# Optimization experiments

Measured on AMD Instinct MI355X. Metric: run time of the kernel, lower is better.

The kernel has to match this reference:

```python
import jax, jax.numpy as jnp
import numpy as np

C_M, C_Z, C = 256, 128, 32
LN_EPS = 1e-5


def setup_inputs() -> dict:
    key = jax.random.key(0)
    ks = jax.random.split(key, 9)
    S, R = 128, 384  # N_seq, N_res
    m = jax.random.normal(ks[0], (S, R, C_M), dtype=jnp.float32)
    ln_g = jnp.ones((C_M,), jnp.float32)
    ln_b = jnp.zeros((C_M,), jnp.float32)
    w1 = jax.random.normal(ks[1], (C_M, C), jnp.float32) / np.sqrt(C_M)
    b1 = jnp.zeros((C,), jnp.float32)
    w2 = jax.random.normal(ks[2], (C_M, C), jnp.float32) / np.sqrt(C_M)
    b2 = jnp.zeros((C,), jnp.float32)
    w_out = jax.random.normal(ks[3], (C * C, C_Z), jnp.float32) / np.sqrt(C * C)
    b_out = jnp.zeros((C_Z,), jnp.float32)
    return {"m": m, "ln_g": ln_g, "ln_b": ln_b, "w1": w1, "b1": b1,
            "w2": w2, "b2": b2, "w_out": w_out, "b_out": b_out}


def reference(m, ln_g, ln_b, w1, b1, w2, b2, w_out, b_out):
    S, R, _ = m.shape
    # LayerNorm over c_m
    mu = jnp.mean(m, axis=-1, keepdims=True)
    var = jnp.var(m, axis=-1, keepdims=True)
    mn = (m - mu) * jax.lax.rsqrt(var + LN_EPS) * ln_g + ln_b
    a = mn @ w1 + b1  # (S, R, c)
    b = mn @ w2 + b2  # (S, R, c)
    # outer product summed over N_seq: out[i,j,x,y] = sum_s a[s,i,x] b[s,j,y]
    o = jnp.einsum('six,sjy->ijxy', a, b)  # (R, R, c, c)
    o = o.reshape(R, R, C * C) @ w_out + b_out  # (R, R, c_z)
    return o / S
```

## Files before the change

### kernel.cpp

```cpp
#include <hip/hip_runtime.h>
#include <hip/hip_bf16.h>

#define R_RES 384
#define S_SEQ 128
#define CM 256
#define CC 32
#define CZ 128

typedef __attribute__((ext_vector_type(8))) short bf16x8;
typedef __attribute__((ext_vector_type(4))) float f32x4;
typedef __attribute__((ext_vector_type(16))) float f32x16;
typedef __attribute__((ext_vector_type(4))) int i32x4;

__device__ __forceinline__ short tobf16(float f) {
    union { __hip_bfloat16 h; short s; } u;
    u.h = __float2bfloat16(f);
    return u.s;
}

__global__ void k_transpose_wout(const float* __restrict__ w_out, short* __restrict__ wbTf) {
    __shared__ float t[64][65];
    int k0 = blockIdx.x * 64;
    int z0 = blockIdx.y * 64;
    int tid = threadIdx.x;
    int c = tid & 63, rg = tid >> 6;
#pragma unroll
    for (int rr = 0; rr < 16; ++rr) {
        int kk = rg * 16 + rr;
        t[kk][c] = w_out[(size_t)(k0 + kk) * CZ + z0 + c];
    }
    __syncthreads();
#pragma unroll
    for (int l = 0; l < 2; ++l) {
        int id = l * 256 + tid;
        int f = id >> 6;
        int ksl = f >> 1, fzl = f & 1;
        int ln = id & 63;
        int zl = fzl * 32 + (ln & 31);
        int kl = ksl * 16 + (ln >> 5) * 8;
        bf16x8 pk;
#pragma unroll
        for (int j = 0; j < 8; ++j) pk[j] = tobf16(t[kl + j][zl]);
        size_t fz = blockIdx.y * 2 + fzl;
        size_t ks16 = blockIdx.x * 4 + ksl;
        *(bf16x8*)(wbTf + ((fz * 64 + ks16) * 64 + ln) * 8) = pk;
    }
}

__global__ void k_pack_w12(const float* __restrict__ w1, const float* __restrict__ w2,
                           short* __restrict__ wcT) {
    int idx = blockIdx.x * 256 + threadIdx.x;
    int k = idx >> 6, n = idx & 63;
    float v = (n < 32) ? w1[k * CC + n] : w2[k * CC + (n - 32)];
    wcT[n * CM + k] = tobf16(v);
}

__global__ __launch_bounds__(256) void k_ln_proj(
    const float* __restrict__ M, const float* __restrict__ ln_g, const float* __restrict__ ln_b,
    const float* __restrict__ b1, const float* __restrict__ b2,
    const short* __restrict__ wcT, short* __restrict__ aTf, short* __restrict__ bTf) {
    __shared__ short mnb[64 * 256];
    __shared__ short ab_s[2][32 * 72];
    int r = blockIdx.x >> 1;
    int s0 = (blockIdx.x & 1) * 64;
    int tid = threadIdx.x, lane = tid & 63, w = tid >> 6;
    int g = lane >> 4, r16 = lane & 15;
    float4 gv = *(const float4*)(ln_g + lane * 4);
    float4 bv = *(const float4*)(ln_b + lane * 4);
    for (int it = 0; it < 16; ++it) {
        int sl = it * 4 + w;
        float4 v = *(const float4*)(M + ((size_t)(s0 + sl) * R_RES + r) * CM + lane * 4);
        float sum = v.x + v.y + v.z + v.w;
        float sq = v.x * v.x + v.y * v.y + v.z * v.z + v.w * v.w;
#pragma unroll
        for (int off = 32; off; off >>= 1) {
            sum += __shfl_xor(sum, off);
            sq  += __shfl_xor(sq, off);
        }
        float mu = sum * (1.0f / 256.0f);
        float var = sq * (1.0f / 256.0f) - mu * mu;
        float rstd = rsqrtf(var + 1e-5f);
        short4 mnp;
        mnp.x = tobf16((v.x - mu) * rstd * gv.x + bv.x);
        mnp.y = tobf16((v.y - mu) * rstd * gv.y + bv.y);
        mnp.z = tobf16((v.z - mu) * rstd * gv.z + bv.z);
        mnp.w = tobf16((v.w - mu) * rstd * gv.w + bv.w);
        int byte = sl * 512 + lane * 8;
        byte ^= ((sl & 7) << 4);
        *(short4*)((char*)mnb + byte) = mnp;
    }
    __syncthreads();
    f32x4 acc[4] = {{0,0,0,0},{0,0,0,0},{0,0,0,0},{0,0,0,0}};
    int srow = w * 16 + r16;
#pragma unroll
    for (int ks = 0; ks < 8; ++ks) {
        int byte = srow * 512 + ks * 64 + g * 16;
        byte ^= ((srow & 7) << 4);
        bf16x8 af = *(const bf16x8*)((const char*)mnb + byte);
#pragma unroll
        for (int nt = 0; nt < 4; ++nt) {
            bf16x8 bf = *(const bf16x8*)(wcT + (nt * 16 + r16) * CM + ks * 32 + g * 8);
            acc[nt] = __builtin_amdgcn_mfma_f32_16x16x32_bf16(af, bf, acc[nt], 0, 0, 0);
        }
    }
#pragma unroll
    for (int nt = 0; nt < 4; ++nt) {
        int n = nt * 16 + r16;
        int x = n & 31, sel = n >> 5;
        float bias = sel ? b2[x] : b1[x];
#pragma unroll
        for (int rr = 0; rr < 4; ++rr) {
            int sl = w * 16 + g * 4 + rr;
            ab_s[sel][x * 72 + sl] = tobf16(acc[nt][rr] + bias);
        }
    }
    __syncthreads();
    int piece = tid >> 6;
    int fl = piece >> 1, kl = piece & 1;
    int ln = tid & 63;
    int x = fl * 16 + (ln & 15);
    int s_loc = kl * 32 + (ln >> 4) * 8;
    i32x4 va = *(const i32x4*)((const char*)ab_s[0] + (x * 72 + s_loc) * 2);
    i32x4 vb = *(const i32x4*)((const char*)ab_s[1] + (x * 72 + s_loc) * 2);
    size_t off = ((((size_t)r * 2 + fl) * 4 + (s0 >> 5) + kl) * 64 + ln) * 16;
    *(i32x4*)((char*)aTf + off) = va;
    *(i32x4*)((char*)bTf + off) = vb;
}

__global__ __launch_bounds__(512, 4) void k_opm(
    const short* __restrict__ aTf, const short* __restrict__ bTf,
    const short* __restrict__ wbTf, const float* __restrict__ b_out,
    float* __restrict__ out) {
    __shared__ __align__(16) char smem[65536];
    int tid = threadIdx.x, lane = tid & 63, w = tid >> 6;
    int g = lane >> 4, r16 = lane & 15;
    int l32 = lane & 31, h = lane >> 5;
    int wm = w & 3, wn = w >> 2;
    int bj = blockIdx.x, bi = blockIdx.y;

    const char* gB = (const char*)bTf + (size_t)bj * 32768;
#pragma unroll
    for (int it = 0; it < 4; ++it) {
        int q = it * 8192 + tid * 16;
        __builtin_amdgcn_global_load_lds(
            (const __attribute__((address_space(1))) void*)(gB + q),
            (__attribute__((address_space(3))) void*)(smem + q), 16, 0, 0);
    }
    __syncthreads();

    f32x4 acc[4][4] = {};
    const char* gA = (const char*)aTf + ((size_t)bi * 16 + wm * 4) * 4096;
#pragma unroll
    for (int ks = 0; ks < 4; ++ks) {
        bf16x8 bf[4], af[4];
#pragma unroll
        for (int ni = 0; ni < 4; ++ni)
            bf[ni] = *(const bf16x8*)(smem + (((wn * 4 + ni) * 4 + ks) * 64 + lane) * 16);
#pragma unroll
        for (int mi = 0; mi < 4; ++mi)
            af[mi] = *(const bf16x8*)(gA + ((mi * 4 + ks) * 64 + lane) * 16);
        __builtin_amdgcn_s_setprio(1);
#pragma unroll
        for (int mi = 0; mi < 4; ++mi)
#pragma unroll
            for (int ni = 0; ni < 4; ++ni)
                acc[mi][ni] = __builtin_amdgcn_mfma_f32_16x16x32_bf16(bf[ni], af[mi], acc[mi][ni], 0, 0, 0);
        __builtin_amdgcn_s_setprio(0);
    }
    __syncthreads();

#pragma unroll
    for (int mi = 0; mi < 4; ++mi)
#pragma unroll
        for (int ni = 0; ni < 4; ++ni) {
            int m = wm * 64 + mi * 16 + r16;
            int nb = wn * 64 + ni * 16 + g * 4;
            int i = m >> 5, x = m & 31;
            int j = nb >> 5, y0 = nb & 31;
            int p = i * 4 + j;
            int byte = (p * 2048 + x * 64 + y0 * 2) ^ (((p & 7) ^ (x & 7)) << 4);
            short4 pk;
            pk.x = tobf16(acc[mi][ni][0]);
            pk.y = tobf16(acc[mi][ni][1]);
            pk.z = tobf16(acc[mi][ni][2]);
            pk.w = tobf16(acc[mi][ni][3]);
            *(short4*)(smem + byte) = pk;
        }
    __syncthreads();

    int kh = w & 1, zq = w >> 1;
    f32x16 c2a = {0,0,0,0,0,0,0,0,0,0,0,0,0,0,0,0};
    f32x16 c2b = {0,0,0,0,0,0,0,0,0,0,0,0,0,0,0,0};
    const short* wbase = wbTf + (size_t)((zq * 64 + kh * 32) * 64) * 8;
#pragma unroll 8
    for (int ks = 0; ks < 32; ++ks) {
        int x = (kh * 32 + ks) >> 1;
        int byte = (l32 * 2048 + kh * 1024 + ks * 32 + h * 16) ^ ((((l32 & 7) ^ (x & 7))) << 4);
        bf16x8 a2f = *(const bf16x8*)(smem + byte);
        bf16x8 wbf = *(const bf16x8*)(wbase + (ks * 64 + lane) * 8);
        if (ks & 1) c2b = __builtin_amdgcn_mfma_f32_32x32x16_bf16(a2f, wbf, c2b, 0, 0, 0);
        else        c2a = __builtin_amdgcn_mfma_f32_32x32x16_bf16(a2f, wbf, c2a, 0, 0, 0);
    }
    f32x16 c2 = c2a + c2b;
    __syncthreads();

#pragma unroll
    for (int q = 0; q < 4; ++q) {
        f32x4 v;
        v[0] = c2[q * 4 + 0]; v[1] = c2[q * 4 + 1];
        v[2] = c2[q * 4 + 2]; v[3] = c2[q * 4 + 3];
        int byte = ((zq * 2 + kh) * 4096 + l32 * 128 + q * 32 + h * 16) ^ ((l32 & 7) << 4);
        *(f32x4*)(smem + byte) = v;
    }
    __syncthreads();

    int z = tid & 127, zq2 = z >> 5, zp = z & 31;
    int pr0 = tid >> 7;
    float bo = b_out[z];
#pragma unroll
    for (int stp = 0; stp < 2; ++stp) {
        int prq = pr0 + stp * 4;
        int base = zq2 * 8192 + zp * 128 + prq * 16;
        int sw = (zp & 7) << 4;
        f32x4 v0 = *(const f32x4*)(smem + (base ^ sw));
        f32x4 v1 = *(const f32x4*)(smem + ((base + 4096) ^ sw));
#pragma unroll
        for (int rr = 0; rr < 4; ++rr) {
            int p = prq * 4 + rr;
            int ig = bi * 8 + (p >> 2);
            int jg = bj * 4 + (p & 3);
            out[((size_t)ig * R_RES + jg) * CZ + z] = (v0[rr] + v1[rr] + bo) * (1.0f / 128.0f);
        }
    }
}

extern "C" void kernel_launch(void* const* d_in, const int* in_sizes, int n_in,
                              void* d_out, int out_size, void* d_ws, size_t ws_size,
                              hipStream_t stream) {
    const float* M     = (const float*)d_in[0];
    const float* ln_g  = (const float*)d_in[1];
    const float* ln_b  = (const float*)d_in[2];
    const float* w1    = (const float*)d_in[3];
    const float* b1    = (const float*)d_in[4];
    const float* w2    = (const float*)d_in[5];
    const float* b2    = (const float*)d_in[6];
    const float* w_out = (const float*)d_in[7];
    const float* b_out = (const float*)d_in[8];
    float* out = (float*)d_out;

    short* aTf  = (short*)d_ws;
    short* bTf  = aTf + 12288 * 128;
    short* wbTf = bTf + 12288 * 128;
    short* wcT  = wbTf + 128 * 1024;

    k_transpose_wout<<<dim3(16, 2), 256, 0, stream>>>(w_out, wbTf);
    k_pack_w12<<<64, 256, 0, stream>>>(w1, w2, wcT);
    k_ln_proj<<<768, 256, 0, stream>>>(M, ln_g, ln_b, b1, b2, wcT, aTf, bTf);
    k_opm<<<dim3(96, 48), 512, 0, stream>>>(aTf, bTf, wbTf, b_out, out);
}
```

Measured before the change: 133.8 us.

## Restructure OPM second GEMM to 16x16 MFMA with K-split and prefetched operands

Changes the w_out packing to 16x32 fragments and rewrites the second GEMM so each wave owns a K quarter and a Z half, using 16x16x32 MFMAs with register double-buffered weight loads. The A fragments of the first GEMM are also prefetched one k-step ahead. Partial sums across the four K quarters are reduced through LDS, and the output is written as vectorized float4 stores. Barriers become explicit lgkmcnt waits. The aim is to hide global load latency and improve store coalescing, at the cost of more registers and an extra LDS reduction.

```diff
diff --git a/kernel.cpp b/kernel.cpp
--- a/kernel.cpp
+++ b/kernel.cpp
@@ -9,13 +9,18 @@
 
 typedef __attribute__((ext_vector_type(8))) short bf16x8;
 typedef __attribute__((ext_vector_type(4))) float f32x4;
-typedef __attribute__((ext_vector_type(16))) float f32x16;
 typedef __attribute__((ext_vector_type(4))) int i32x4;
 
 __device__ __forceinline__ short tobf16(float f) {
     union { __hip_bfloat16 h; short s; } u;
     u.h = __float2bfloat16(f);
     return u.s;
+}
+
+__device__ __forceinline__ void lgkm_barrier() {
+    asm volatile("s_waitcnt lgkmcnt(0)" ::: "memory");
+    __builtin_amdgcn_s_barrier();
+    __builtin_amdgcn_sched_barrier(0);
 }
 
 __global__ void k_transpose_wout(const float* __restrict__ w_out, short* __restrict__ wbTf) {
@@ -34,16 +39,16 @@
     for (int l = 0; l < 2; ++l) {
         int id = l * 256 + tid;
         int f = id >> 6;
-        int ksl = f >> 1, fzl = f & 1;
+        int z16l = f >> 1, k32l = f & 1;
         int ln = id & 63;
-        int zl = fzl * 32 + (ln & 31);
-        int kl = ksl * 16 + (ln >> 5) * 8;
+        int zl = z16l * 16 + (ln & 15);
+        int kl = k32l * 32 + (ln >> 4) * 8;
         bf16x8 pk;
 #pragma unroll
         for (int j = 0; j < 8; ++j) pk[j] = tobf16(t[kl + j][zl]);
-        size_t fz = blockIdx.y * 2 + fzl;
-        size_t ks16 = blockIdx.x * 4 + ksl;
-        *(bf16x8*)(wbTf + ((fz * 64 + ks16) * 64 + ln) * 8) = pk;
+        int z16 = blockIdx.y * 4 + z16l;
+        int k32 = blockIdx.x * 2 + k32l;
+        *(bf16x8*)(wbTf + ((size_t)(z16 * 32 + k32) * 64 + ln) * 8) = pk;
     }
 }
 
@@ -134,7 +139,6 @@
     __shared__ __align__(16) char smem[65536];
     int tid = threadIdx.x, lane = tid & 63, w = tid >> 6;
     int g = lane >> 4, r16 = lane & 15;
-    int l32 = lane & 31, h = lane >> 5;
     int wm = w & 3, wn = w >> 2;
     int bj = blockIdx.x, bi = blockIdx.y;
 
@@ -146,37 +150,48 @@
             (const __attribute__((address_space(1))) void*)(gB + q),
             (__attribute__((address_space(3))) void*)(smem + q), 16, 0, 0);
     }
+    const char* gA = (const char*)aTf + (size_t)bi * 65536;
+    bf16x8 afc[4];
+#pragma unroll
+    for (int mi = 0; mi < 4; ++mi)
+        afc[mi] = *(const bf16x8*)(gA + ((wm * 4 + mi) * 4 + 0) * 1024 + lane * 16);
+    asm volatile("s_waitcnt vmcnt(0)" ::: "memory");
     __syncthreads();
 
     f32x4 acc[4][4] = {};
-    const char* gA = (const char*)aTf + ((size_t)bi * 16 + wm * 4) * 4096;
 #pragma unroll
     for (int ks = 0; ks < 4; ++ks) {
-        bf16x8 bf[4], af[4];
+        bf16x8 bf[4], afn[4];
 #pragma unroll
         for (int ni = 0; ni < 4; ++ni)
             bf[ni] = *(const bf16x8*)(smem + (((wn * 4 + ni) * 4 + ks) * 64 + lane) * 16);
+        if (ks < 3) {
+#pragma unroll
+            for (int mi = 0; mi < 4; ++mi)
+                afn[mi] = *(const bf16x8*)(gA + ((wm * 4 + mi) * 4 + ks + 1) * 1024 + lane * 16);
+        }
+        __builtin_amdgcn_s_setprio(1);
 #pragma unroll
         for (int mi = 0; mi < 4; ++mi)
-            af[mi] = *(const bf16x8*)(gA + ((mi * 4 + ks) * 64 + lane) * 16);
-        __builtin_amdgcn_s_setprio(1);
-#pragma unroll
-        for (int mi = 0; mi < 4; ++mi)
 #pragma unroll
             for (int ni = 0; ni < 4; ++ni)
-                acc[mi][ni] = __builtin_amdgcn_mfma_f32_16x16x32_bf16(bf[ni], af[mi], acc[mi][ni], 0, 0, 0);
+                acc[mi][ni] = __builtin_amdgcn_mfma_f32_16x16x32_bf16(bf[ni], afc[mi], acc[mi][ni], 0, 0, 0);
         __builtin_amdgcn_s_setprio(0);
-    }
-    __syncthreads();
+        if (ks < 3) {
+#pragma unroll
+            for (int mi = 0; mi < 4; ++mi) afc[mi] = afn[mi];
+        }
+    }
+    lgkm_barrier();
 
 #pragma unroll
     for (int mi = 0; mi < 4; ++mi)
 #pragma unroll
         for (int ni = 0; ni < 4; ++ni) {
-            int m = wm * 64 + mi * 16 + r16;
-            int nb = wn * 64 + ni * 16 + g * 4;
-            int i = m >> 5, x = m & 31;
-            int j = nb >> 5, y0 = nb & 31;
+            int fm = wm * 4 + mi;
+            int fn = wn * 4 + ni;
+            int i = fm >> 1, x = (fm & 1) * 16 + r16;
+            int j = fn >> 1, y0 = (fn & 1) * 16 + g * 4;
             int p = i * 4 + j;
             int byte = (p * 2048 + x * 64 + y0 * 2) ^ (((p & 7) ^ (x & 7)) << 4);
             short4 pk;
@@ -186,51 +201,88 @@
             pk.w = tobf16(acc[mi][ni][3]);
             *(short4*)(smem + byte) = pk;
         }
-    __syncthreads();
-
-    int kh = w & 1, zq = w >> 1;
-    f32x16 c2a = {0,0,0,0,0,0,0,0,0,0,0,0,0,0,0,0};
-    f32x16 c2b = {0,0,0,0,0,0,0,0,0,0,0,0,0,0,0,0};
-    const short* wbase = wbTf + (size_t)((zq * 64 + kh * 32) * 64) * 8;
-#pragma unroll 8
-    for (int ks = 0; ks < 32; ++ks) {
-        int x = (kh * 32 + ks) >> 1;
-        int byte = (l32 * 2048 + kh * 1024 + ks * 32 + h * 16) ^ ((((l32 & 7) ^ (x & 7))) << 4);
-        bf16x8 a2f = *(const bf16x8*)(smem + byte);
-        bf16x8 wbf = *(const bf16x8*)(wbase + (ks * 64 + lane) * 8);
-        if (ks & 1) c2b = __builtin_amdgcn_mfma_f32_32x32x16_bf16(a2f, wbf, c2b, 0, 0, 0);
-        else        c2a = __builtin_amdgcn_mfma_f32_32x32x16_bf16(a2f, wbf, c2a, 0, 0, 0);
-    }
-    f32x16 c2 = c2a + c2b;
-    __syncthreads();
-
-#pragma unroll
-    for (int q = 0; q < 4; ++q) {
-        f32x4 v;
-        v[0] = c2[q * 4 + 0]; v[1] = c2[q * 4 + 1];
-        v[2] = c2[q * 4 + 2]; v[3] = c2[q * 4 + 3];
-        int byte = ((zq * 2 + kh) * 4096 + l32 * 128 + q * 32 + h * 16) ^ ((l32 & 7) << 4);
-        *(f32x4*)(smem + byte) = v;
-    }
-    __syncthreads();
-
-    int z = tid & 127, zq2 = z >> 5, zp = z & 31;
-    int pr0 = tid >> 7;
-    float bo = b_out[z];
-#pragma unroll
-    for (int stp = 0; stp < 2; ++stp) {
-        int prq = pr0 + stp * 4;
-        int base = zq2 * 8192 + zp * 128 + prq * 16;
-        int sw = (zp & 7) << 4;
-        f32x4 v0 = *(const f32x4*)(smem + (base ^ sw));
-        f32x4 v1 = *(const f32x4*)(smem + ((base + 4096) ^ sw));
-#pragma unroll
-        for (int rr = 0; rr < 4; ++rr) {
-            int p = prq * 4 + rr;
-            int ig = bi * 8 + (p >> 2);
-            int jg = bj * 4 + (p & 3);
-            out[((size_t)ig * R_RES + jg) * CZ + z] = (v0[rr] + v1[rr] + bo) * (1.0f / 128.0f);
-        }
+
+    int zh = w & 1, kq = w >> 1;
+    bf16x8 wcur[4], wnxt[4];
+#pragma unroll
+    for (int zi = 0; zi < 4; ++zi)
+        wcur[zi] = *(const bf16x8*)(wbTf +
+            ((size_t)((zh * 4 + zi) * 32 + kq * 8 + 0) * 64 + lane) * 8);
+    lgkm_barrier();
+
+    f32x4 c[2][4] = {};
+#pragma unroll
+    for (int kk = 0; kk < 8; ++kk) {
+        int ks = kq * 8 + kk;
+        if (kk < 7) {
+#pragma unroll
+            for (int zi = 0; zi < 4; ++zi)
+                wnxt[zi] = *(const bf16x8*)(wbTf +
+                    ((size_t)((zh * 4 + zi) * 32 + ks + 1) * 64 + lane) * 8);
+        }
+        bf16x8 a2f[2];
+#pragma unroll
+        for (int pf = 0; pf < 2; ++pf) {
+            int p = pf * 16 + r16;
+            int byte = (p * 2048 + ks * 64 + g * 16) ^ ((((p & 7) ^ (ks & 7))) << 4);
+            a2f[pf] = *(const bf16x8*)(smem + byte);
+        }
+        __builtin_amdgcn_s_setprio(1);
+#pragma unroll
+        for (int zi = 0; zi < 4; ++zi) {
+            c[0][zi] = __builtin_amdgcn_mfma_f32_16x16x32_bf16(a2f[0], wcur[zi], c[0][zi], 0, 0, 0);
+            c[1][zi] = __builtin_amdgcn_mfma_f32_16x16x32_bf16(a2f[1], wcur[zi], c[1][zi], 0, 0, 0);
+        }
+        __builtin_amdgcn_s_setprio(0);
+        if (kk < 7) {
+#pragma unroll
+            for (int zi = 0; zi < 4; ++zi) wcur[zi] = wnxt[zi];
+        }
+    }
+    lgkm_barrier();
+
+#pragma unroll
+    for (int pf = 0; pf < 2; ++pf)
+#pragma unroll
+        for (int zi = 0; zi < 4; ++zi)
+#pragma unroll
+            for (int rr = 0; rr < 4; ++rr) {
+                int p = pf * 16 + g * 4 + rr;
+                int z = zh * 64 + zi * 16 + r16;
+                int byte = (kq * 16384 + p * 512 + z * 4) ^ ((p & 7) << 4);
+                *(float*)(smem + byte) = c[pf][zi][rr];
+            }
+    lgkm_barrier();
+
+    {
+        int p = tid >> 4;
+        int z0 = (tid & 15) * 8;
+        int sw = (p & 7) << 4;
+        f32x4 s0 = {0, 0, 0, 0}, s1 = {0, 0, 0, 0};
+#pragma unroll
+        for (int q = 0; q < 4; ++q) {
+            int base = q * 16384 + p * 512 + z0 * 4;
+            f32x4 u0 = *(const f32x4*)(smem + (base ^ sw));
+            f32x4 u1 = *(const f32x4*)(smem + ((base + 16) ^ sw));
+            s0 += u0;
+            s1 += u1;
+        }
+        float4 bo0 = *(const float4*)(b_out + z0);
+        float4 bo1 = *(const float4*)(b_out + z0 + 4);
+        f32x4 r0, r1;
+        r0[0] = (s0[0] + bo0.x) * (1.0f / 128.0f);
+        r0[1] = (s0[1] + bo0.y) * (1.0f / 128.0f);
+        r0[2] = (s0[2] + bo0.z) * (1.0f / 128.0f);
+        r0[3] = (s0[3] + bo0.w) * (1.0f / 128.0f);
+        r1[0] = (s1[0] + bo1.x) * (1.0f / 128.0f);
+        r1[1] = (s1[1] + bo1.y) * (1.0f / 128.0f);
+        r1[2] = (s1[2] + bo1.z) * (1.0f / 128.0f);
+        r1[3] = (s1[3] + bo1.w) * (1.0f / 128.0f);
+        int ig = bi * 8 + (p >> 2);
+        int jg = bj * 4 + (p & 3);
+        float* po = out + ((size_t)ig * R_RES + jg) * CZ + z0;
+        *(f32x4*)(po) = r0;
+        *(f32x4*)(po + 4) = r1;
     }
 }
 
```

Result: no change. 131.6 us (-1.7%).
